# Kernel optimization log

Hardware: AMD Instinct MI355X
Metric: run time of the kernel (lower is better)

The kernel has to match this reference:

```python
import jax, jax.numpy as jnp
import numpy as np

IN_DIM, OUT_DIM = 256, 10
N_EXPERTS, N_MEM, STEPS, N_SUB, MAX_K = 12, 32, 6, 5, 5
EXPERT_DIMS = [2048, 2560, 3072, 3584, 4096, 2304, 2816, 3328, 3840, 4608, 3072, 4096]
MAX_E = 4608
N_ITEMS = 4096
SCALE = IN_DIM ** -0.5

def _gelu(x):
    return jax.nn.gelu(x, approximate=False)

_ACTS = [jax.nn.silu, _gelu, lambda x: x * jnp.tanh(jax.nn.softplus(x)), jax.nn.relu,
         jax.nn.selu, jnp.tanh, jax.nn.softplus, jax.nn.elu]
EXPERT_ACTS = [_ACTS[i % 8] for i in range(N_EXPERTS)]

def _ln(x, s, b, eps=1e-5):
    mu = jnp.mean(x, -1, keepdims=True)
    var = jnp.mean((x - mu) ** 2, -1, keepdims=True)
    return (x - mu) * jax.lax.rsqrt(var + eps) * s + b

def _cell(x, ln_s, ln_b, w1, b1, w2, b2):
    h = _gelu(_ln(x, ln_s, ln_b) @ w1.T + b1)
    return x + h @ w2.T + b2

def _ctx_attn(cur, bank, qw, kw, vw):
    q = cur @ qw.T
    k = bank @ kw.T
    v = bank @ vw.T
    attn = jax.nn.softmax(jnp.einsum('nd,ntd->nt', q, k) * SCALE, axis=-1)
    return jnp.einsum('nt,ntd->nd', attn, v)

def _renorm_sparse_topk(probs, active_k):
    tv, ti = jax.lax.top_k(probs, MAX_K)
    mask = (jnp.arange(MAX_K)[None, :] < active_k[:, None]).astype(probs.dtype)
    vals = tv * mask
    rows = jnp.arange(probs.shape[0])[:, None]
    sparse = jnp.zeros_like(probs).at[rows, ti].set(vals)
    return sparse / jnp.maximum(jnp.sum(sparse, -1, keepdims=True), 1e-6)

def _fwd(x, W, b,
         shared_up_w, shared_down_w, shared_ln_s, shared_ln_b, shared_scale,
         mem_keys, mem_vals, mem_q_w, mem_out_w, mem_wg_w, mem_wg_b, mem_wv_w, mem_wv_b,
         depth_q_w, depth_k_w, depth_v_w, depth_out_w,
         rc_ln_s, rc_ln_b, rc_w1, rc_b1, rc_w2, rc_b2,
         ssm_in_w, ssm_out_w, ssm_decay,
         sub_w, sub_b, gate_w, gate_b,
         budget_w, budget_b,
         exp_up, exp_down, exp_ln_s, exp_ln_b,
         halt_w, halt_b,
         aux_up_w, aux_down_w, aux_ln_s, aux_ln_b, aux_gate_w, aux_gate_b,
         rf_ln_s, rf_ln_b, rf_w1, rf_b1, rf_w2, rf_b2, reflect_out_w,
         coll_q_w, coll_k_w, coll_v_w, coll_out_w,
         revisit_w, revisit_b,
         vc_ln_s, vc_ln_b, vc_w1, vc_b1, vc_w2, vc_b2,
         ver_q_w, ver_k_w, ver_v_w, ver_out_w, ver_gate_w, ver_gate_b, correction_out_w,
         mix):
    n = x.shape[0]
    base = x @ W.T + b
    shared = _ln(jax.nn.silu(x @ shared_up_w.T) @ shared_down_w.T, shared_ln_s, shared_ln_b)
    aux = _ln(_gelu(x @ aux_up_w.T) @ aux_down_w.T, aux_ln_s, aux_ln_b)

    mem_vals_b = jnp.broadcast_to(mem_vals[None], (n, N_MEM, IN_DIM))
    current = x
    mem_logits = jnp.zeros_like(base)
    depth_logits = jnp.zeros_like(base)
    cum_halt = jnp.zeros((n, 1), x.dtype)
    bank = []
    for s in range(STEPS):
        q = current @ mem_q_w.T
        attn = jax.nn.softmax((q @ mem_keys.T) * SCALE, axis=-1)
        mem_read = jnp.einsum('ns,nsd->nd', attn, mem_vals_b)
        wg = jax.nn.sigmoid(jnp.concatenate([current, mem_read], -1) @ mem_wg_w.T + mem_wg_b)
        wv = current @ mem_wv_w.T + mem_wv_b
        mem_vals_b = mem_vals_b * (1.0 - wg[..., None]) + wg[..., None] * wv[:, None, :]
        if bank:
            depth_ctx = _ctx_attn(current, jnp.stack(bank, 1), depth_q_w, depth_k_w, depth_v_w)
        else:
            depth_ctx = jnp.zeros_like(current)
        current = _cell(current + mem_read + depth_ctx,
                        rc_ln_s[s], rc_ln_b[s], rc_w1[s], rc_b1[s], rc_w2[s], rc_b2[s])
        h = jnp.tanh(current @ ssm_in_w.T) * jax.nn.sigmoid(ssm_decay)
        current = current + h @ ssm_out_w.T
        bank.append(current)
        halt = jax.nn.sigmoid((current @ halt_w[s])[:, None] + halt_b[s])
        w_step = (1.0 - cum_halt) * halt
        mem_logits = mem_logits + w_step * (mem_read @ mem_out_w.T)
        depth_logits = depth_logits + w_step * (depth_ctx @ depth_out_w.T)
        cum_halt = jnp.minimum(cum_halt + halt, 1.0)

    sub_logits = jnp.einsum('nd,sed->nse', current, sub_w) + sub_b
    sub_probs = jax.nn.softmax(sub_logits, axis=-1)
    gate = jax.nn.softmax(current @ gate_w.T + gate_b, axis=-1)
    probs = jnp.einsum('ns,nse->ne', gate, sub_probs)
    active_k = jnp.argmax(current @ budget_w.T + budget_b, axis=-1) + 1
    sparse = _renorm_sparse_topk(probs, active_k)

    expert_out = jnp.zeros_like(base)
    for i in range(N_EXPERTS):
        h = EXPERT_ACTS[i](current @ exp_up[i].T)
        o = _ln(h @ exp_down[i].T, exp_ln_s[i], exp_ln_b[i])
        expert_out = expert_out + sparse[:, i:i + 1] * o

    r = current
    for i in range(3):
        r = _cell(r, rf_ln_s[i], rf_ln_b[i], rf_w1[i], rf_b1[i], rf_w2[i], rf_b2[i])
    reflect_logits = r @ reflect_out_w.T

    stack = jnp.stack(bank, 1)
    coll_ctx = _ctx_attn(current, stack, coll_q_w, coll_k_w, coll_v_w)
    coll_logits = coll_ctx @ coll_out_w.T
    revisit = jax.nn.sigmoid(jnp.concatenate([x, current, coll_ctx], -1) @ revisit_w.T + revisit_b)

    v = current
    for i in range(2):
        v = _cell(v, vc_ln_s[i], vc_ln_b[i], vc_w1[i], vc_b1[i], vc_w2[i], vc_b2[i])
    ver_ctx = _ctx_attn(v, stack, ver_q_w, ver_k_w, ver_v_w)
    vg = jax.nn.softmax(jnp.concatenate([v, ver_ctx], -1) @ ver_gate_w.T + ver_gate_b, axis=-1)
    ver_logits = ver_ctx @ ver_out_w.T
    corr_logits = v @ correction_out_w.T

    ag = jax.nn.softmax(x @ aux_gate_w.T + aux_gate_b, axis=-1)
    alpha, beta, gamma, delta, eps_, zeta = [jnp.tanh(mix[i]) for i in range(6)]
    logits = (base
              + shared_scale * (ag[:, :1] * shared + ag[:, 1:] * aux)
              + alpha * expert_out
              + beta * mem_logits + zeta * depth_logits
              + gamma * reflect_logits
              + delta * revisit * coll_logits
              + eps_ * (vg[:, :1] * ver_logits + vg[:, 1:] * corr_logits))
    return logits


def setup_inputs() -> dict:
    key = jax.random.key(0)
    ks = iter(jax.random.split(key, 128))
    def nrm(shape, std=0.02):
        return jax.random.normal(next(ks), shape, jnp.float32) * std
    d, o = IN_DIM, OUT_DIM
    inp = dict(
        x=jax.random.normal(next(ks), (N_ITEMS, d), jnp.float32),
        W=nrm((o, d), 0.05), b=jnp.zeros((o,), jnp.float32),
        shared_up_w=nrm((3072, d)), shared_down_w=nrm((o, 3072)),
        shared_ln_s=jnp.ones((o,)), shared_ln_b=jnp.zeros((o,)),
        shared_scale=jnp.float32(1.0),
        mem_keys=nrm((N_MEM, d)), mem_vals=nrm((N_MEM, d)),
        mem_q_w=nrm((d, d), 0.01), mem_out_w=nrm((o, d), 0.01),
        mem_wg_w=nrm((N_MEM, 2 * d), 0.01), mem_wg_b=jnp.zeros((N_MEM,)),
        mem_wv_w=nrm((d, d), 0.01), mem_wv_b=jnp.zeros((d,)),
        depth_q_w=nrm((d, d), 0.01), depth_k_w=nrm((d, d), 0.01),
        depth_v_w=nrm((d, d), 0.01), depth_out_w=nrm((o, d), 0.01),
        rc_ln_s=jnp.ones((STEPS, d)), rc_ln_b=jnp.zeros((STEPS, d)),
        rc_w1=nrm((STEPS, 896, d)), rc_b1=jnp.zeros((STEPS, 896)),
        rc_w2=nrm((STEPS, d, 896)), rc_b2=jnp.zeros((STEPS, d)),
        ssm_in_w=nrm((48, d)), ssm_out_w=nrm((d, 48)), ssm_decay=jnp.zeros((48,)),
        sub_w=nrm((N_SUB, N_EXPERTS, d)), sub_b=jnp.zeros((N_SUB, N_EXPERTS)),
        gate_w=nrm((N_SUB, d)), gate_b=jnp.zeros((N_SUB,)),
        budget_w=nrm((MAX_K, d), 0.01), budget_b=jnp.zeros((MAX_K,)),
        halt_w=nrm((STEPS, d), 0.01), halt_b=jnp.full((STEPS,), -2.0, jnp.float32),
        aux_up_w=nrm((4096, d)), aux_down_w=nrm((o, 4096)),
        aux_ln_s=jnp.ones((o,)), aux_ln_b=jnp.zeros((o,)),
        aux_gate_w=nrm((2, d), 0.01), aux_gate_b=jnp.zeros((2,)),
        rf_ln_s=jnp.ones((3, d)), rf_ln_b=jnp.zeros((3, d)),
        rf_w1=nrm((3, 1280, d)), rf_b1=jnp.zeros((3, 1280)),
        rf_w2=nrm((3, d, 1280)), rf_b2=jnp.zeros((3, d)),
        reflect_out_w=nrm((o, d), 0.01),
        coll_q_w=nrm((d, d), 0.01), coll_k_w=nrm((d, d), 0.01),
        coll_v_w=nrm((d, d), 0.01), coll_out_w=nrm((o, d), 0.01),
        revisit_w=nrm((1, 3 * d), 0.01), revisit_b=jnp.zeros((1,)),
        vc_ln_s=jnp.ones((2, d)), vc_ln_b=jnp.zeros((2, d)),
        vc_w1=nrm((2, 1536, d)), vc_b1=jnp.zeros((2, 1536)),
        vc_w2=nrm((2, d, 1536)), vc_b2=jnp.zeros((2, d)),
        ver_q_w=nrm((d, d), 0.01), ver_k_w=nrm((d, d), 0.01),
        ver_v_w=nrm((d, d), 0.01), ver_out_w=nrm((o, d), 0.01),
        ver_gate_w=nrm((2, 2 * d), 0.01), ver_gate_b=jnp.zeros((2,)),
        correction_out_w=nrm((o, d), 0.01),
        mix=jnp.full((6,), 0.5, jnp.float32),
    )
    up = jax.random.normal(next(ks), (N_EXPERTS, MAX_E, d), jnp.float32) * 0.02
    down = jax.random.normal(next(ks), (N_EXPERTS, o, MAX_E), jnp.float32) * 0.01
    col = jnp.arange(MAX_E)
    dims = jnp.array(EXPERT_DIMS)
    mask = (col[None, :] < dims[:, None]).astype(jnp.float32)
    inp['exp_up'] = up * mask[:, :, None]
    inp['exp_down'] = down * mask[:, None, :]
    inp['exp_ln_s'] = jnp.ones((N_EXPERTS, o))
    inp['exp_ln_b'] = jnp.zeros((N_EXPERTS, o))
    return inp


def reference(x, W, b,
              shared_up_w, shared_down_w, shared_ln_s, shared_ln_b, shared_scale,
              mem_keys, mem_vals, mem_q_w, mem_out_w, mem_wg_w, mem_wg_b, mem_wv_w, mem_wv_b,
              depth_q_w, depth_k_w, depth_v_w, depth_out_w,
              rc_ln_s, rc_ln_b, rc_w1, rc_b1, rc_w2, rc_b2,
              ssm_in_w, ssm_out_w, ssm_decay,
              sub_w, sub_b, gate_w, gate_b,
              budget_w, budget_b,
              exp_up, exp_down, exp_ln_s, exp_ln_b,
              halt_w, halt_b,
              aux_up_w, aux_down_w, aux_ln_s, aux_ln_b, aux_gate_w, aux_gate_b,
              rf_ln_s, rf_ln_b, rf_w1, rf_b1, rf_w2, rf_b2, reflect_out_w,
              coll_q_w, coll_k_w, coll_v_w, coll_out_w,
              revisit_w, revisit_b,
              vc_ln_s, vc_ln_b, vc_w1, vc_b1, vc_w2, vc_b2,
              ver_q_w, ver_k_w, ver_v_w, ver_out_w, ver_gate_w, ver_gate_b, correction_out_w,
              mix):
    return _fwd(x, W, b,
                shared_up_w, shared_down_w, shared_ln_s, shared_ln_b, shared_scale,
                mem_keys, mem_vals, mem_q_w, mem_out_w, mem_wg_w, mem_wg_b, mem_wv_w, mem_wv_b,
                depth_q_w, depth_k_w, depth_v_w, depth_out_w,
                rc_ln_s, rc_ln_b, rc_w1, rc_b1, rc_w2, rc_b2,
                ssm_in_w, ssm_out_w, ssm_decay,
                sub_w, sub_b, gate_w, gate_b,
                budget_w, budget_b,
                exp_up, exp_down, exp_ln_s, exp_ln_b,
                halt_w, halt_b,
                aux_up_w, aux_down_w, aux_ln_s, aux_ln_b, aux_gate_w, aux_gate_b,
                rf_ln_s, rf_ln_b, rf_w1, rf_b1, rf_w2, rf_b2, reflect_out_w,
                coll_q_w, coll_k_w, coll_v_w, coll_out_w,
                revisit_w, revisit_b,
                vc_ln_s, vc_ln_b, vc_w1, vc_b1, vc_w2, vc_b2,
                ver_q_w, ver_k_w, ver_v_w, ver_out_w, ver_gate_w, ver_gate_b, correction_out_w,
                mix)
```

## Files before the change

### kernel.cpp

```cpp
#include <hip/hip_runtime.h>


constexpr int NI      = 4096;
constexpr int DIM     = 256;
constexpr int ODIM    = 10;
constexpr int NMEM_   = 32;
constexpr int NSTEPS_ = 6;
constexpr int NEXPERT_= 12;
constexpr int MAXE    = 4608;
constexpr int TOTCOL  = 46592;
#define SCL 0.0625f

__constant__ int GCNT[14] = {8,10,12,14,16,9,11,13,15,18,12,16,12,16};
__constant__ int CCNT[14] = {32,40,48,56,64,36,44,52,60,72,48,64,48,64};
__constant__ int ZCOL[14] = {0,2048,4608,7680,11264,15360,17664,20480,
                             23808,27648,32256,35328,39424,42496};

typedef __attribute__((ext_vector_type(8))) short short8v;
typedef __attribute__((ext_vector_type(4))) float float4v;
typedef __attribute__((ext_vector_type(4))) unsigned short ushort4v;


__device__ __forceinline__ float wred_sum(float v){
  #pragma unroll
  for (int m = 32; m > 0; m >>= 1) v += __shfl_xor(v, m, 64);
  return v;
}
__device__ __forceinline__ float wred_max(float v){
  #pragma unroll
  for (int m = 32; m > 0; m >>= 1) v = fmaxf(v, __shfl_xor(v, m, 64));
  return v;
// ... 7 lines not shown
    case 1: return geluf(x);
    case 2: return x*tanhf(softplusf(x));
    case 3: return fmaxf(x,0.f);
    case 4: { const float l=1.0507009873554805f, al=1.6732632423543772f;
              return x>0.f ? l*x : l*al*expm1f(x); }
    case 5: return tanhf(x);
    case 6: return softplusf(x);
    default: return x>0.f ? x : expm1f(x);
  }
}
__device__ __forceinline__ unsigned short f2b(float f){
  unsigned u = __float_as_uint(f);
  u = u + 0x7FFFu + ((u >> 16) & 1u);
  return (unsigned short)(u >> 16);
}
__device__ __forceinline__ float dot256f(const float* __restrict__ a,
                                         const float* __restrict__ w, float s){
  for (int k = 0; k < DIM; k += 4){
    float4 av = *(const float4*)&a[k];
    float4 wv = *(const float4*)&w[k];
    s = fmaf(av.x,wv.x, fmaf(av.y,wv.y, fmaf(av.z,wv.z, fmaf(av.w,wv.w, s))));
  }
  return s;
}
__device__ __forceinline__ void ln10(const float* p, const float* s, const float* b, float* o){
  float mu = 0.f;
  #pragma unroll
  for (int i=0;i<ODIM;i++) mu += p[i];
  mu *= 0.1f;
  float var = 0.f;
// ... 32 lines not shown
  int t = threadIdx.x;
  int c = t >> 3, kb = (t & 7)*32;
  const float* srow = src + (size_t)(colbase + c)*DIM + kb;
  #pragma unroll
  for (int j = 0; j < 4; j++){
    float4 f0 = *(const float4*)&srow[j*8];
    float4 f1 = *(const float4*)&srow[j*8+4];
    short8v s;
    s[0]=(short)f2b(f0.x); s[1]=(short)f2b(f0.y); s[2]=(short)f2b(f0.z); s[3]=(short)f2b(f0.w);
    s[4]=(short)f2b(f1.x); s[5]=(short)f2b(f1.y); s[6]=(short)f2b(f1.z); s[7]=(short)f2b(f1.w);
    int kq = (t & 7)*4 + j;
    *(short8v*)&dst[((size_t)kq*64 + c)*8] = s;
  }
}

template<int EPI>
__global__ __launch_bounds__(256)
void gemm_k(const float* __restrict__ A, const float* __restrict__ W,
            const float* __restrict__ bias, const float* __restrict__ R,
            float* __restrict__ C, int N, int K)
{
  __shared__ float As[32][68];
  __shared__ float Ws[32][68];
  const int bm = blockIdx.y*64, bn = blockIdx.x*64;
  const int tid = threadIdx.x;
  const int tx = tid & 15, ty = tid >> 4;
  const int lrow = tid >> 2, lkq = (tid & 3) * 8;
  float acc[4][4] = {};
  for (int k0 = 0; k0 < K; k0 += 32){
    #pragma unroll
    for (int h = 0; h < 2; ++h){
      int kk = lkq + h*4;
      float4 va = make_float4(0.f,0.f,0.f,0.f), vw = make_float4(0.f,0.f,0.f,0.f);
      if (k0 + kk < K)
        va = *(const float4*)&A[(size_t)(bm+lrow)*K + k0 + kk];
      if (bn + lrow < N && k0 + kk < K)
        vw = *(const float4*)&W[(size_t)(bn+lrow)*K + k0 + kk];
      As[kk+0][lrow]=va.x; As[kk+1][lrow]=va.y; As[kk+2][lrow]=va.z; As[kk+3][lrow]=va.w;
      Ws[kk+0][lrow]=vw.x; Ws[kk+1][lrow]=vw.y; Ws[kk+2][lrow]=vw.z; Ws[kk+3][lrow]=vw.w;
    }
    __syncthreads();
    #pragma unroll
    for (int kk = 0; kk < 32; ++kk){
      float4 a4 = *(const float4*)&As[kk][ty*4];
      float4 b4 = *(const float4*)&Ws[kk][tx*4];
      float av[4] = {a4.x,a4.y,a4.z,a4.w};
      float bv[4] = {b4.x,b4.y,b4.z,b4.w};
      #pragma unroll
      for (int i=0;i<4;i++)
        #pragma unroll
        for (int j=0;j<4;j++) acc[i][j] = fmaf(av[i], bv[j], acc[i][j]);
    }
    __syncthreads();
  }
  #pragma unroll
  for (int i=0;i<4;i++){
    int r = bm + ty*4 + i;
    #pragma unroll
    for (int j=0;j<4;j++){
      int c = bn + tx*4 + j;
      if (c >= N) continue;
      float v = acc[i][j];
      if constexpr (EPI==1) v += bias[c];
      else if constexpr (EPI==2) v = geluf(v + bias[c]);
      else if constexpr (EPI==3) v = v + bias[c] + R[(size_t)r*N + c];
      C[(size_t)r*N + c] = v;
    }
  }
}

template<int EPI>
__global__ __launch_bounds__(256)
void bgemm_k(const short* __restrict__ A, const short* __restrict__ B,
             const float* __restrict__ bias, const float* __restrict__ R,
             float* __restrict__ Cf, unsigned short* __restrict__ Cb,
             int N, int K)
{
  __shared__ short As[128][40];
  __shared__ short Bsm[64][40];
  const int bm = blockIdx.y*128, bn = blockIdx.x*64;
  const int tid = threadIdx.x;
// ... 35 lines not shown
      for (int reg = 0; reg < 4; reg++){
        int row = bm + wave*32 + mt*16 + lg*4 + reg;
        int col = bn + nt*16 + l15;
        float v = acc[mt][nt][reg];
        if constexpr (EPI==0){
          v = geluf(v + bias[col]);
          Cb[(size_t)row*N + col] = f2b(v);
        } else {
          v = v + bias[col] + R[(size_t)row*N + col];
          Cf[(size_t)row*N + col] = v;
        }
      }
}

__global__ __launch_bounds__(512)
void moe2_k(const float* __restrict__ cur, const float* __restrict__ x,
            const float* __restrict__ exp_up, const float* __restrict__ shared_up,
            const float* __restrict__ aux_up, const short* __restrict__ upb,
            const float* __restrict__ exp_down, const float* __restrict__ shared_down,
            const float* __restrict__ aux_down,
            float* __restrict__ expert_pre, float* __restrict__ shared_pre,
            float* __restrict__ aux_pre)
{
  __shared__ short Bs[16384];
  __shared__ float Ds[64][12];
  int gy = blockIdx.y, z = 0;
  while (gy >= GCNT[z]){ gy -= GCNT[z]; z++; }
  const int localcol = gy*256;
  int act, dstride; const float* upf; const float* down; float* outp;
  if (z < NEXPERT_){
    act = z & 7;
    upf = exp_up + (size_t)z*MAXE*DIM;
    down = exp_down + (size_t)z*ODIM*MAXE; dstride = MAXE;
    outp = expert_pre + (size_t)z*NI*ODIM;
  } else if (z == NEXPERT_){
    act = 0; upf = shared_up; down = shared_down; dstride = 3072; outp = shared_pre;
  } else {
    act = 1; upf = aux_up; down = aux_down; dstride = 4096; outp = aux_pre;
  }
  const float* X = (z < NEXPERT_) ? cur : x;
  const int bm = blockIdx.x*128;
  const int tid = threadIdx.x, wave = tid >> 6, lane = tid & 63;
  const int l15 = lane & 15, lg = lane >> 4;

  short8v afrag[8];
  {
    const float* xr = X + (size_t)(bm + wave*16 + l15)*DIM;
    #pragma unroll
    for (int ks = 0; ks < 8; ks++){
      float4 v0 = *(const float4*)&xr[ks*32 + lg*8];
      float4 v1 = *(const float4*)&xr[ks*32 + lg*8 + 4];
      short8v a;
      a[0]=(short)f2b(v0.x); a[1]=(short)f2b(v0.y); a[2]=(short)f2b(v0.z); a[3]=(short)f2b(v0.w);
      a[4]=(short)f2b(v1.x); a[5]=(short)f2b(v1.y); a[6]=(short)f2b(v1.z); a[7]=(short)f2b(v1.w);
      afrag[ks] = a;
    }
  }
  float racc[4][10];
  #pragma unroll
  for (int r = 0; r < 4; r++)
    #pragma unroll
    for (int o = 0; o < 10; o++) racc[r][o] = 0.f;

  const int sc = tid & 63, sw = tid >> 6;
  const int gchunk0 = (ZCOL[z] + localcol) >> 6;
  for (int ch = 0; ch < 4; ch++){
    const int cb = localcol + ch*64;
    __syncthreads();
    if (upb){
      const short* chunk = upb + ((size_t)(gchunk0 + ch))*16384;
      #pragma unroll
      for (int i = 0; i < 4; i++){
        int u = tid + 512*i;
        short8v v = *(const short8v*)&chunk[(size_t)u*8];
        int c = u & 63, kq = u >> 6;
        int byteoff = ((c << 9) + (kq << 4)) ^ ((c & 7) << 4);
        *(short8v*)((char*)Bs + byteoff) = v;
      }
    } else {
      const float* srow = upf + (size_t)(cb + sc)*DIM;
      #pragma unroll
      for (int i = 0; i < 4; i++){
        int kq = sw + 8*i;
        float4 f0 = *(const float4*)&srow[kq*8];
        float4 f1 = *(const float4*)&srow[kq*8 + 4];
        short8v s;
        s[0]=(short)f2b(f0.x); s[1]=(short)f2b(f0.y); s[2]=(short)f2b(f0.z); s[3]=(short)f2b(f0.w);
        s[4]=(short)f2b(f1.x); s[5]=(short)f2b(f1.y); s[6]=(short)f2b(f1.z); s[7]=(short)f2b(f1.w);
        int byteoff = ((sc << 9) + (kq << 4)) ^ ((sc & 7) << 4);
        *(short8v*)((char*)Bs + byteoff) = s;
      }
    }
    for (int t2 = tid; t2 < 640; t2 += 512){
      int e = t2 & 63, o = t2 >> 6;
      Ds[e][o] = down[(size_t)o*dstride + cb + e];
    }
    __syncthreads();

    float4v acc[4] = {};
    #pragma unroll
    for (int ks = 0; ks < 8; ks++){
      #pragma unroll
      for (int nt = 0; nt < 4; nt++){
        int c = nt*16 + l15, kq = ks*4 + lg;
        int byteoff = ((c << 9) + (kq << 4)) ^ ((c & 7) << 4);
        short8v b = *(const short8v*)((const char*)Bs + byteoff);
        acc[nt] = __builtin_amdgcn_mfma_f32_16x16x32_bf16(afrag[ks], b, acc[nt], 0, 0, 0);
      }
    }
    #pragma unroll
    for (int nt = 0; nt < 4; nt++){
      const float* dp = &Ds[nt*16 + l15][0];
      float4 d0 = *(const float4*)dp;
      float4 d1 = *(const float4*)(dp + 4);
      float  d8 = dp[8], d9 = dp[9];
      float dv[10] = {d0.x,d0.y,d0.z,d0.w,d1.x,d1.y,d1.z,d1.w,d8,d9};
      float hv[4];
      #pragma unroll
      for (int reg = 0; reg < 4; reg++) hv[reg] = act_apply(act, acc[nt][reg]);
      #pragma unroll
      for (int o = 0; o < 10; o++)
        #pragma unroll
        for (int reg = 0; reg < 4; reg++)
          racc[reg][o] = fmaf(hv[reg], dv[o], racc[reg][o]);
    }
  }
  #pragma unroll
  for (int reg = 0; reg < 4; reg++)
    #pragma unroll
    for (int o = 0; o < 10; o++){
      float v = racc[reg][o];
      v += __shfl_xor(v, 1, 64); v += __shfl_xor(v, 2, 64);
      v += __shfl_xor(v, 4, 64); v += __shfl_xor(v, 8, 64);
      racc[reg][o] = v;
    }
  if (l15 == 0){
    #pragma unroll
    for (int reg = 0; reg < 4; reg++){
      int row = bm + wave*16 + lg*4 + reg;
      #pragma unroll
      for (int o = 0; o < 10; o++)
        atomicAdd(&outp[(size_t)row*ODIM + o], racc[reg][o]);
    }
  }
}

__global__ void atb_k(const float* __restrict__ A, const float* __restrict__ B,
                      float* __restrict__ C, int M, int I, int J)
{
  int idx = blockIdx.x*256 + threadIdx.x;
  if (idx >= I*J) return;
  int i = idx / J, j = idx - i*J;
  float s = 0.f;
  for (int m = 0; m < M; m++) s = fmaf(A[(size_t)m*I+i], B[(size_t)m*J+j], s);
  C[idx] = s;
}
__global__ void ab_k(const float* __restrict__ A, const float* __restrict__ B,
                     float* __restrict__ C, int M, int K, int N)
{
// ... 369 lines not shown
  #pragma unroll
  for (int o = 0; o < ODIM; o++){
    size_t ix = (size_t)item*ODIM + o;
    float v = base10[ix]
      + ss*(ag0*sh[o] + ag1*axl[o])
      + al*eo[o]
      + be*mem_logits[ix] + ze*depth_logits[ix]
      + ga*reflect10[ix]
      + de*rv*coll10[ix]
      + ep*(vg0*ver10[ix] + vg1*corr10[ix]);
    out[ix] = v;
  }
}


static void launch_gemm(int epi, const float* A, const float* W, const float* b,
                        const float* R, float* C, int N, int K, hipStream_t stream)
{
  dim3 g((N+63)/64, NI/64), blk(256);
  switch(epi){
    case 0: gemm_k<0><<<g,blk,0,stream>>>(A,W,b,R,C,N,K); break;
    case 1: gemm_k<1><<<g,blk,0,stream>>>(A,W,b,R,C,N,K); break;
    case 2: gemm_k<2><<<g,blk,0,stream>>>(A,W,b,R,C,N,K); break;
    case 3: gemm_k<3><<<g,blk,0,stream>>>(A,W,b,R,C,N,K); break;
  }
}

static void launch_cvt(const float* in, unsigned short* out, size_t n, hipStream_t stream)
{
  cvt_k<<<(unsigned)((n/4 + 255)/256), 256, 0, stream>>>(in, out, (int)n);
}

extern "C" void kernel_launch(void* const* d_in, const int* in_sizes, int n_in,
                              void* d_out, int out_size, void* d_ws, size_t ws_size,
                              hipStream_t stream)
{
  (void)in_sizes; (void)n_in; (void)out_size;
  const float* x             = (const float*)d_in[0];
  const float* Wm            = (const float*)d_in[1];
  const float* bvec          = (const float*)d_in[2];
  const float* shared_up_w   = (const float*)d_in[3];
  const float* shared_down_w = (const float*)d_in[4];
  const float* shared_ln_s   = (const float*)d_in[5];
  const float* shared_ln_b   = (const float*)d_in[6];
  const float* shared_scale  = (const float*)d_in[7];
  const float* mem_keys      = (const float*)d_in[8];
  const float* mem_vals      = (const float*)d_in[9];
  const float* mem_q_w       = (const float*)d_in[10];
  const float* mem_out_w     = (const float*)d_in[11];
  const float* mem_wg_w      = (const float*)d_in[12];
  const float* mem_wg_b      = (const float*)d_in[13];
  const float* mem_wv_w      = (const float*)d_in[14];
// ... 50 lines not shown
  const float* ver_out_w     = (const float*)d_in[65];
  const float* ver_gate_w    = (const float*)d_in[66];
  const float* ver_gate_b    = (const float*)d_in[67];
  const float* correction_out_w = (const float*)d_in[68];
  const float* mix           = (const float*)d_in[69];
  const float* exp_up        = (const float*)d_in[70];
  const float* exp_down      = (const float*)d_in[71];
  const float* exp_ln_s      = (const float*)d_in[72];
  const float* exp_ln_b      = (const float*)d_in[73];
  float* out = (float*)d_out;

  float* w = (float*)d_ws;
  size_t off = 0;
  auto WS = [&](size_t nf){ float* p = w + off; off += nf; return p; };
  float* bank      = WS((size_t)NSTEPS_*NI*DIM);
  float* cur_in    = WS((size_t)NI*DIM);
  float* t_ln      = WS((size_t)NI*DIM);
  float* hbig      = WS((size_t)NI*896);
  float* mem_read  = WS((size_t)NI*DIM);
  float* depth_ctx = WS((size_t)NI*DIM);
  float* q2        = WS((size_t)NI*DIM);
  float* wsumb     = WS((size_t)NI*DIM);
  float* wv_hist   = WS((size_t)NSTEPS_*NI*DIM);
  float* a_state   = WS((size_t)NI*NMEM_);
  float* c_state   = WS((size_t)NI*NMEM_*NSTEPS_);
  float* rbuf      = WS((size_t)NI*DIM);
  float* vbuf      = WS((size_t)NI*DIM);
  float* coll_ctx  = WS((size_t)NI*DIM);
  float* ver_ctx   = WS((size_t)NI*DIM);
  float* sparse    = WS((size_t)NI*NEXPERT_);
  float* base10    = WS((size_t)NI*ODIM);
  float* reflect10 = WS((size_t)NI*ODIM);
  float* coll10    = WS((size_t)NI*ODIM);
  float* ver10     = WS((size_t)NI*ODIM);
  float* corr10    = WS((size_t)NI*ODIM);
  float* PdT       = WS((size_t)DIM*DIM);
  float* PcT       = WS((size_t)DIM*DIM);
  float* PvT       = WS((size_t)DIM*DIM);
  float* MK        = WS((size_t)NMEM_*DIM);
  float* zbase     = w + off;
  float* mem_logits   = WS((size_t)NI*ODIM);
  float* depth_logits = WS((size_t)NI*ODIM);
  float* shared_pre   = WS((size_t)NI*ODIM);
  float* aux_pre      = WS((size_t)NI*ODIM);
  float* expert_pre   = WS((size_t)NEXPERT_*NI*ODIM);
  float* cum_halt     = WS((size_t)NI);
  size_t zbytes = (size_t)((w + off) - zbase) * sizeof(float);
  hipMemsetAsync((void*)zbase, 0, zbytes, stream);

  unsigned short* bb = (unsigned short*)(w + off);
  size_t boff = 0;
  auto BS = [&](size_t ns){ unsigned short* p = bb + boff; boff += ns; return p; };
  unsigned short* t_ln_b = BS((size_t)NI*DIM);
  unsigned short* rfw1b  = BS((size_t)3*1280*DIM);
  unsigned short* rfw2b  = BS((size_t)3*DIM*1280);
  unsigned short* vcw1b  = BS((size_t)2*1536*DIM);
  unsigned short* vcw2b  = BS((size_t)2*DIM*1536);
  unsigned short* upb    = bb + boff;
  size_t upb_n = (size_t)TOTCOL*DIM;
  size_t base_bytes = off*sizeof(float) + boff*sizeof(unsigned short);
  bool use_upb = (ws_size >= base_bytes + upb_n*sizeof(unsigned short));
  unsigned short* hb = (unsigned short*)hbig;

  launch_cvt(rf_w1, rfw1b, (size_t)3*1280*DIM, stream);
  launch_cvt(rf_w2, rfw2b, (size_t)3*DIM*1280, stream);
  launch_cvt(vc_w1, vcw1b, (size_t)2*1536*DIM, stream);
  launch_cvt(vc_w2, vcw2b, (size_t)2*DIM*1536, stream);
  if (use_upb)
    cvtup_k<<<TOTCOL/64, 512, 0, stream>>>(exp_up, shared_up_w, aux_up_w, (short*)upb);

  atb_k<<<(DIM*DIM+255)/256, 256, 0, stream>>>(depth_k_w, depth_q_w, PdT, DIM, DIM, DIM);
  atb_k<<<(DIM*DIM+255)/256, 256, 0, stream>>>(coll_k_w,  coll_q_w,  PcT, DIM, DIM, DIM);
  atb_k<<<(DIM*DIM+255)/256, 256, 0, stream>>>(ver_k_w,   ver_q_w,   PvT, DIM, DIM, DIM);
  ab_k <<<(NMEM_*DIM+255)/256, 256, 0, stream>>>(mem_keys, mem_q_w, MK, NMEM_, DIM, DIM);

  const float* cur = x;
  for (int s = 0; s < NSTEPS_; s++){
    memread2_k<<<NI/4, 256, 0, stream>>>(cur, MK, a_state, c_state, mem_vals,
                                         wv_hist, mem_read, s);
    memwrite_k<<<NI/4, 256, 0, stream>>>(cur, mem_read, mem_wg_w, mem_wg_b,
                                         a_state, c_state, s);
    launch_gemm(1, cur, mem_wv_w, mem_wv_b, nullptr,
                wv_hist + (size_t)s*NI*DIM, DIM, DIM, stream);
    if (s > 0){
      launch_gemm(0, cur, PdT, nullptr, nullptr, q2, DIM, DIM, stream);
      bankattn_k<<<NI/4, 256, 0, stream>>>(q2, bank, wsumb, s);
      launch_gemm(0, wsumb, depth_v_w, nullptr, nullptr, depth_ctx, DIM, DIM, stream);
    }
    ln3_k<<<NI/4, 256, 0, stream>>>(cur, mem_read, (s > 0 ? depth_ctx : nullptr),
                                    rc_ln_s + (size_t)s*DIM, rc_ln_b + (size_t)s*DIM,
                                    cur_in, t_ln, nullptr);
    launch_gemm(2, t_ln, rc_w1 + (size_t)s*896*DIM, rc_b1 + (size_t)s*896,
                nullptr, hbig, 896, DIM, stream);
    launch_gemm(3, hbig, rc_w2 + (size_t)s*DIM*896, rc_b2 + (size_t)s*DIM,
                cur_in, cur_in, DIM, 896, stream);
    float* newcur = bank + (size_t)s*NI*DIM;
    ssmhalt_k<<<NI/4, 256, 0, stream>>>(cur_in, mem_read, depth_ctx,
                                        ssm_in_w, ssm_out_w, ssm_decay,
                                        halt_w, halt_b, mem_out_w, depth_out_w,
                                        newcur, mem_logits, depth_logits, cum_halt, s);
    cur = newcur;
  }

  router2_k<<<NI/4, 256, 0, stream>>>(cur, sub_w, sub_b, gate_w, gate_b,
                                      budget_w, budget_b, sparse);

  moe2_k<<<dim3(NI/128, 182), 512, 0, stream>>>(
      cur, x, exp_up, shared_up_w, aux_up_w, use_upb ? (const short*)upb : nullptr,
      exp_down, shared_down_w, aux_down_w, expert_pre, shared_pre, aux_pre);

  const float* rsrc = cur;
  for (int i = 0; i < 3; i++){
    ln3_k<<<NI/4, 256, 0, stream>>>(rsrc, nullptr, nullptr,
                                    rf_ln_s + (size_t)i*DIM, rf_ln_b + (size_t)i*DIM,
                                    nullptr, nullptr, t_ln_b);
    bgemm_k<0><<<dim3(1280/64, NI/128), 256, 0, stream>>>(
        (const short*)t_ln_b, (const short*)(rfw1b + (size_t)i*1280*DIM),
        rf_b1 + (size_t)i*1280, nullptr, nullptr, hb, 1280, DIM);
    bgemm_k<1><<<dim3(DIM/64, NI/128), 256, 0, stream>>>(
        (const short*)hb, (const short*)(rfw2b + (size_t)i*DIM*1280),
        rf_b2 + (size_t)i*DIM, rsrc, rbuf, nullptr, DIM, 1280);
    rsrc = rbuf;
  }

  const float* vsrc = cur;
  for (int i = 0; i < 2; i++){
    ln3_k<<<NI/4, 256, 0, stream>>>(vsrc, nullptr, nullptr,
                                    vc_ln_s + (size_t)i*DIM, vc_ln_b + (size_t)i*DIM,
                                    nullptr, nullptr, t_ln_b);
    bgemm_k<0><<<dim3(1536/64, NI/128), 256, 0, stream>>>(
        (const short*)t_ln_b, (const short*)(vcw1b + (size_t)i*1536*DIM),
        vc_b1 + (size_t)i*1536, nullptr, nullptr, hb, 1536, DIM);
    bgemm_k<1><<<dim3(DIM/64, NI/128), 256, 0, stream>>>(
        (const short*)hb, (const short*)(vcw2b + (size_t)i*DIM*1536),
        vc_b2 + (size_t)i*DIM, vsrc, vbuf, nullptr, DIM, 1536);
    vsrc = vbuf;
  }

  launch_gemm(0, cur, PcT, nullptr, nullptr, q2, DIM, DIM, stream);
  bankattn_k<<<NI/4, 256, 0, stream>>>(q2, bank, wsumb, NSTEPS_);
  launch_gemm(0, wsumb, coll_v_w, nullptr, nullptr, coll_ctx, DIM, DIM, stream);

  launch_gemm(0, vbuf, PvT, nullptr, nullptr, q2, DIM, DIM, stream);
  bankattn_k<<<NI/4, 256, 0, stream>>>(q2, bank, wsumb, NSTEPS_);
  launch_gemm(0, wsumb, ver_v_w, nullptr, nullptr, ver_ctx, DIM, DIM, stream);

  heads_k<<<(NI*50 + 255)/256, 256, 0, stream>>>(
      rbuf, coll_ctx, ver_ctx, vbuf, x,
      reflect_out_w, coll_out_w, ver_out_w, correction_out_w, Wm, bvec,
      reflect10, coll10, ver10, corr10, base10);

  final_k<<<(NI+255)/256, 256, 0, stream>>>(
      x, cur, vbuf, coll_ctx, ver_ctx,
      base10, shared_pre, aux_pre, expert_pre, sparse,
      mem_logits, depth_logits, reflect10, coll10, ver10, corr10,
      shared_ln_s, shared_ln_b, aux_ln_s, aux_ln_b, exp_ln_s, exp_ln_b,
      aux_gate_w, aux_gate_b, ver_gate_w, ver_gate_b, revisit_w, revisit_b,
      shared_scale, mix, out);
}
```

Before: 3.360 ms.

## Enlarge fp32 GEMM tiles, fuse wv/depth-query GEMMs, pipeline MoE and drop atomics

Replaces the 64x64 fp32 GEMM with a 128-row tiled kernel using 8xTN register blocking. The mem_wv and depth-query projections are fused into one 512-wide GEMM over concatenated weights. The MoE kernel now reads pre-converted bf16 activations, always uses the bf16 up-weight buffer, and double-buffers chunk loads in registers. Its atomicAdd accumulation is replaced by bf16 partial sums plus a separate reduction kernel. The workspace is reorganised so buffers overlap, which risks aliasing, and storing partials in bf16 loses some precision.

```diff
diff --git a/kernel.cpp b/kernel.cpp
--- a/kernel.cpp
+++ b/kernel.cpp
@@ -9,12 +9,14 @@
 constexpr int NEXPERT_= 12;
 constexpr int MAXE    = 4608;
 constexpr int TOTCOL  = 46592;
+constexpr int NGRP    = 182;
 #define SCL 0.0625f
 
-__constant__ int GCNT[14] = {8,10,12,14,16,9,11,13,15,18,12,16,12,16};
-__constant__ int CCNT[14] = {32,40,48,56,64,36,44,52,60,72,48,64,48,64};
-__constant__ int ZCOL[14] = {0,2048,4608,7680,11264,15360,17664,20480,
-                             23808,27648,32256,35328,39424,42496};
+__constant__ int GCNT[14]   = {8,10,12,14,16,9,11,13,15,18,12,16,12,16};
+__constant__ int GSTART[14] = {0,8,18,30,44,60,69,80,93,108,126,138,154,166};
+__constant__ int CCNT[14]   = {32,40,48,56,64,36,44,52,60,72,48,64,48,64};
+__constant__ int ZCOL[14]   = {0,2048,4608,7680,11264,15360,17664,20480,
+                               23808,27648,32256,35328,39424,42496};
 
 typedef __attribute__((ext_vector_type(8))) short short8v;
 typedef __attribute__((ext_vector_type(4))) float float4v;
@@ -52,6 +54,9 @@
   u = u + 0x7FFFu + ((u >> 16) & 1u);
   return (unsigned short)(u >> 16);
 }
+__device__ __forceinline__ float b2f(unsigned short u){
+  return __uint_as_float((unsigned)u << 16);
+}
 __device__ __forceinline__ float dot256f(const float* __restrict__ a,
                                          const float* __restrict__ w, float s){
   for (int k = 0; k < DIM; k += 4){
@@ -114,57 +119,85 @@
   }
 }
 
-template<int EPI>
+template<int EPI, int BN>
 __global__ __launch_bounds__(256)
-void gemm_k(const float* __restrict__ A, const float* __restrict__ W,
-            const float* __restrict__ bias, const float* __restrict__ R,
-            float* __restrict__ C, int N, int K)
-{
-  __shared__ float As[32][68];
-  __shared__ float Ws[32][68];
-  const int bm = blockIdx.y*64, bn = blockIdx.x*64;
+void gemm128_k(const float* __restrict__ A, const float* __restrict__ W,
+               const float* __restrict__ bias, const float* __restrict__ R,
+               float* __restrict__ C, float* __restrict__ C2, int N, int K)
+{
+  __shared__ float As[32][132];
+  __shared__ float Bs[32][BN==128?132:68];
+  const int bm = blockIdx.y*128, bn = blockIdx.x*BN;
   const int tid = threadIdx.x;
   const int tx = tid & 15, ty = tid >> 4;
-  const int lrow = tid >> 2, lkq = (tid & 3) * 8;
-  float acc[4][4] = {};
+  constexpr int TN = BN/16;
+  float acc[8][TN] = {};
+  const int arow = tid >> 1, ak = (tid & 1)*16;
+  const int brow = tid >> 2, bk = (tid & 3)*8;
   for (int k0 = 0; k0 < K; k0 += 32){
-    #pragma unroll
-    for (int h = 0; h < 2; ++h){
-      int kk = lkq + h*4;
-      float4 va = make_float4(0.f,0.f,0.f,0.f), vw = make_float4(0.f,0.f,0.f,0.f);
-      if (k0 + kk < K)
-        va = *(const float4*)&A[(size_t)(bm+lrow)*K + k0 + kk];
-      if (bn + lrow < N && k0 + kk < K)
-        vw = *(const float4*)&W[(size_t)(bn+lrow)*K + k0 + kk];
-      As[kk+0][lrow]=va.x; As[kk+1][lrow]=va.y; As[kk+2][lrow]=va.z; As[kk+3][lrow]=va.w;
-      Ws[kk+0][lrow]=vw.x; Ws[kk+1][lrow]=vw.y; Ws[kk+2][lrow]=vw.z; Ws[kk+3][lrow]=vw.w;
+    float4 a[4];
+    #pragma unroll
+    for (int i=0;i<4;i++) a[i] = *(const float4*)&A[(size_t)(bm+arow)*K + k0 + ak + 4*i];
+    float4 b[4];
+    if constexpr (BN==128){
+      #pragma unroll
+      for (int i=0;i<4;i++) b[i] = *(const float4*)&W[(size_t)(bn+arow)*K + k0 + ak + 4*i];
+    } else {
+      #pragma unroll
+      for (int i=0;i<2;i++) b[i] = *(const float4*)&W[(size_t)(bn+brow)*K + k0 + bk + 4*i];
     }
     __syncthreads();
     #pragma unroll
-    for (int kk = 0; kk < 32; ++kk){
-      float4 a4 = *(const float4*)&As[kk][ty*4];
-      float4 b4 = *(const float4*)&Ws[kk][tx*4];
-      float av[4] = {a4.x,a4.y,a4.z,a4.w};
-      float bv[4] = {b4.x,b4.y,b4.z,b4.w};
-      #pragma unroll
-      for (int i=0;i<4;i++)
+    for (int i=0;i<4;i++){
+      As[ak+4*i+0][arow]=a[i].x; As[ak+4*i+1][arow]=a[i].y;
+      As[ak+4*i+2][arow]=a[i].z; As[ak+4*i+3][arow]=a[i].w;
+    }
+    if constexpr (BN==128){
+      #pragma unroll
+      for (int i=0;i<4;i++){
+        Bs[ak+4*i+0][arow]=b[i].x; Bs[ak+4*i+1][arow]=b[i].y;
+        Bs[ak+4*i+2][arow]=b[i].z; Bs[ak+4*i+3][arow]=b[i].w;
+      }
+    } else {
+      #pragma unroll
+      for (int i=0;i<2;i++){
+        Bs[bk+4*i+0][brow]=b[i].x; Bs[bk+4*i+1][brow]=b[i].y;
+        Bs[bk+4*i+2][brow]=b[i].z; Bs[bk+4*i+3][brow]=b[i].w;
+      }
+    }
+    __syncthreads();
+    #pragma unroll
+    for (int kk=0;kk<32;kk++){
+      float a8[8];
+      *(float4*)&a8[0] = *(const float4*)&As[kk][ty*8];
+      *(float4*)&a8[4] = *(const float4*)&As[kk][ty*8+4];
+      float b8[TN];
+      if constexpr (TN==8){
+        *(float4*)&b8[0] = *(const float4*)&Bs[kk][tx*8];
+        *(float4*)&b8[4] = *(const float4*)&Bs[kk][tx*8+4];
+      } else {
+        *(float4*)&b8[0] = *(const float4*)&Bs[kk][tx*4];
+      }
+      #pragma unroll
+      for (int i=0;i<8;i++)
         #pragma unroll
-        for (int j=0;j<4;j++) acc[i][j] = fmaf(av[i], bv[j], acc[i][j]);
-    }
-    __syncthreads();
-  }
-  #pragma unroll
-  for (int i=0;i<4;i++){
-    int r = bm + ty*4 + i;
-    #pragma unroll
-    for (int j=0;j<4;j++){
-      int c = bn + tx*4 + j;
-      if (c >= N) continue;
+        for (int j=0;j<TN;j++) acc[i][j] = fmaf(a8[i], b8[j], acc[i][j]);
+    }
+  }
+  #pragma unroll
+  for (int i=0;i<8;i++){
+    int r = bm + ty*8 + i;
+    #pragma unroll
+    for (int j=0;j<TN;j++){
+      int c = bn + tx*TN + j;
       float v = acc[i][j];
-      if constexpr (EPI==1) v += bias[c];
-      else if constexpr (EPI==2) v = geluf(v + bias[c]);
-      else if constexpr (EPI==3) v = v + bias[c] + R[(size_t)r*N + c];
-      C[(size_t)r*N + c] = v;
+      if constexpr (EPI==0){ C[(size_t)r*N + c] = v; }
+      else if constexpr (EPI==2){ C[(size_t)r*N + c] = geluf(v + bias[c]); }
+      else if constexpr (EPI==3){ C[(size_t)r*N + c] = v + bias[c] + R[(size_t)r*N + c]; }
+      else if constexpr (EPI==6){
+        if (c < 256) C[(size_t)r*256 + c] = v + bias[c];
+        else C2[(size_t)r*256 + (c-256)] = v;
+      }
     }
   }
 }
@@ -230,47 +263,32 @@
 }
 
 __global__ __launch_bounds__(512)
-void moe2_k(const float* __restrict__ cur, const float* __restrict__ x,
-            const float* __restrict__ exp_up, const float* __restrict__ shared_up,
-            const float* __restrict__ aux_up, const short* __restrict__ upb,
+void moe3_k(const unsigned short* __restrict__ curb, const unsigned short* __restrict__ xb,
+            const short* __restrict__ upb,
             const float* __restrict__ exp_down, const float* __restrict__ shared_down,
             const float* __restrict__ aux_down,
-            float* __restrict__ expert_pre, float* __restrict__ shared_pre,
-            float* __restrict__ aux_pre)
+            unsigned short* __restrict__ part)
 {
   __shared__ short Bs[16384];
   __shared__ float Ds[64][12];
-  int gy = blockIdx.y, z = 0;
+  const int g = blockIdx.y;
+  int gy = g, z = 0;
   while (gy >= GCNT[z]){ gy -= GCNT[z]; z++; }
   const int localcol = gy*256;
-  int act, dstride; const float* upf; const float* down; float* outp;
-  if (z < NEXPERT_){
-    act = z & 7;
-    upf = exp_up + (size_t)z*MAXE*DIM;
-    down = exp_down + (size_t)z*ODIM*MAXE; dstride = MAXE;
-    outp = expert_pre + (size_t)z*NI*ODIM;
-  } else if (z == NEXPERT_){
-    act = 0; upf = shared_up; down = shared_down; dstride = 3072; outp = shared_pre;
-  } else {
-    act = 1; upf = aux_up; down = aux_down; dstride = 4096; outp = aux_pre;
-  }
-  const float* X = (z < NEXPERT_) ? cur : x;
+  int act, dstride; const float* down;
+  if (z < 12){ act = z & 7; down = exp_down + (size_t)z*ODIM*MAXE; dstride = MAXE; }
+  else if (z == 12){ act = 0; down = shared_down; dstride = 3072; }
+  else { act = 1; down = aux_down; dstride = 4096; }
+  const unsigned short* X = (z < 12) ? curb : xb;
   const int bm = blockIdx.x*128;
   const int tid = threadIdx.x, wave = tid >> 6, lane = tid & 63;
   const int l15 = lane & 15, lg = lane >> 4;
 
   short8v afrag[8];
-  {
-    const float* xr = X + (size_t)(bm + wave*16 + l15)*DIM;
-    #pragma unroll
-    for (int ks = 0; ks < 8; ks++){
-      float4 v0 = *(const float4*)&xr[ks*32 + lg*8];
-      float4 v1 = *(const float4*)&xr[ks*32 + lg*8 + 4];
-      short8v a;
-      a[0]=(short)f2b(v0.x); a[1]=(short)f2b(v0.y); a[2]=(short)f2b(v0.z); a[3]=(short)f2b(v0.w);
-      a[4]=(short)f2b(v1.x); a[5]=(short)f2b(v1.y); a[6]=(short)f2b(v1.z); a[7]=(short)f2b(v1.w);
-      afrag[ks] = a;
-    }
+  { const unsigned short* xr = X + (size_t)(bm + wave*16 + l15)*DIM;
+    #pragma unroll
+    for (int ks = 0; ks < 8; ks++)
+      afrag[ks] = *(const short8v*)&xr[ks*32 + lg*8];
   }
   float racc[4][10];
   #pragma unroll
@@ -278,44 +296,44 @@
     #pragma unroll
     for (int o = 0; o < 10; o++) racc[r][o] = 0.f;
 
-  const int sc = tid & 63, sw = tid >> 6;
   const int gchunk0 = (ZCOL[z] + localcol) >> 6;
+  const int dso = tid >> 6, dse = tid & 63;
+
+  auto ld = [&](int ch, short8v* p, float& d0, float& d1){
+    const short* chunk = upb + ((size_t)(gchunk0 + ch))*16384;
+    #pragma unroll
+    for (int i = 0; i < 4; i++)
+      p[i] = *(const short8v*)&chunk[(size_t)(tid + 512*i)*8];
+    int cb = localcol + ch*64;
+    d0 = down[(size_t)dso*dstride + cb + dse];
+    d1 = (tid < 128) ? down[(size_t)(dso+8)*dstride + cb + dse] : 0.f;
+  };
+
+  short8v preA[4], preB[4];
+  float dA0, dA1, dB0, dB1;
+  ld(0, preA, dA0, dA1);
+  #pragma unroll
   for (int ch = 0; ch < 4; ch++){
-    const int cb = localcol + ch*64;
+    const short8v* P = (ch & 1) ? preB : preA;
+    float d0 = (ch & 1) ? dB0 : dA0;
+    float d1 = (ch & 1) ? dB1 : dA1;
+    #pragma unroll
+    for (int i = 0; i < 4; i++){
+      int u = tid + 512*i;
+      int c = u & 63, kq = u >> 6;
+      int byteoff = ((c << 9) + (kq << 4)) ^ ((c & 7) << 4);
+      *(short8v*)((char*)Bs + byteoff) = P[i];
+    }
+    Ds[dse][dso] = d0;
+    if (tid < 128) Ds[dse][dso + 8] = d1;
     __syncthreads();
-    if (upb){
-      const short* chunk = upb + ((size_t)(gchunk0 + ch))*16384;
-      #pragma unroll
-      for (int i = 0; i < 4; i++){
-        int u = tid + 512*i;
-        short8v v = *(const short8v*)&chunk[(size_t)u*8];
-        int c = u & 63, kq = u >> 6;
-        int byteoff = ((c << 9) + (kq << 4)) ^ ((c & 7) << 4);
-        *(short8v*)((char*)Bs + byteoff) = v;
-      }
-    } else {
-      const float* srow = upf + (size_t)(cb + sc)*DIM;
-      #pragma unroll
-      for (int i = 0; i < 4; i++){
-        int kq = sw + 8*i;
-        float4 f0 = *(const float4*)&srow[kq*8];
-        float4 f1 = *(const float4*)&srow[kq*8 + 4];
-        short8v s;
-        s[0]=(short)f2b(f0.x); s[1]=(short)f2b(f0.y); s[2]=(short)f2b(f0.z); s[3]=(short)f2b(f0.w);
-        s[4]=(short)f2b(f1.x); s[5]=(short)f2b(f1.y); s[6]=(short)f2b(f1.z); s[7]=(short)f2b(f1.w);
-        int byteoff = ((sc << 9) + (kq << 4)) ^ ((sc & 7) << 4);
-        *(short8v*)((char*)Bs + byteoff) = s;
-      }
-    }
-    for (int t2 = tid; t2 < 640; t2 += 512){
-      int e = t2 & 63, o = t2 >> 6;
-      Ds[e][o] = down[(size_t)o*dstride + cb + e];
-    }
-    __syncthreads();
-
+    if (ch < 3){
+      if (ch & 1) ld(ch + 1, preA, dA0, dA1);
+      else        ld(ch + 1, preB, dB0, dB1);
+    }
     float4v acc[4] = {};
     #pragma unroll
-    for (int ks = 0; ks < 8; ks++){
+    for (int ks = 0; ks < 8; ks++)
       #pragma unroll
       for (int nt = 0; nt < 4; nt++){
         int c = nt*16 + l15, kq = ks*4 + lg;
@@ -323,14 +341,13 @@
         short8v b = *(const short8v*)((const char*)Bs + byteoff);
         acc[nt] = __builtin_amdgcn_mfma_f32_16x16x32_bf16(afrag[ks], b, acc[nt], 0, 0, 0);
       }
-    }
     #pragma unroll
     for (int nt = 0; nt < 4; nt++){
       const float* dp = &Ds[nt*16 + l15][0];
-      float4 d0 = *(const float4*)dp;
-      float4 d1 = *(const float4*)(dp + 4);
+      float4 dv0 = *(const float4*)dp;
+      float4 dv1 = *(const float4*)(dp + 4);
       float  d8 = dp[8], d9 = dp[9];
-      float dv[10] = {d0.x,d0.y,d0.z,d0.w,d1.x,d1.y,d1.z,d1.w,d8,d9};
+      float dv[10] = {dv0.x,dv0.y,dv0.z,dv0.w,dv1.x,dv1.y,dv1.z,dv1.w,d8,d9};
       float hv[4];
       #pragma unroll
       for (int reg = 0; reg < 4; reg++) hv[reg] = act_apply(act, acc[nt][reg]);
@@ -340,6 +357,7 @@
         for (int reg = 0; reg < 4; reg++)
           racc[reg][o] = fmaf(hv[reg], dv[o], racc[reg][o]);
     }
+    __syncthreads();
   }
   #pragma unroll
   for (int reg = 0; reg < 4; reg++)
@@ -356,9 +374,25 @@
       int row = bm + wave*16 + lg*4 + reg;
       #pragma unroll
       for (int o = 0; o < 10; o++)
-        atomicAdd(&outp[(size_t)row*ODIM + o], racc[reg][o]);
-    }
-  }
+        part[((size_t)g*NI + row)*ODIM + o] = f2b(racc[reg][o]);
+    }
+  }
+}
+
+__global__ __launch_bounds__(256)
+void red_k(const unsigned short* __restrict__ part, float* __restrict__ expert_pre,
+           float* __restrict__ shared_pre, float* __restrict__ aux_pre)
+{
+  int idx = blockIdx.x*256 + threadIdx.x;
+  if (idx >= 14*NI*ODIM) return;
+  int z = idx / (NI*ODIM), rem = idx - z*NI*ODIM;
+  float s = 0.f;
+  int g0 = GSTART[z], gn = GCNT[z];
+  for (int g2 = 0; g2 < gn; g2++)
+    s += b2f(part[(size_t)(g0 + g2)*NI*ODIM + rem]);
+  if (z < 12) expert_pre[(size_t)z*NI*ODIM + rem] = s;
+  else if (z == 12) shared_pre[rem] = s;
+  else aux_pre[rem] = s;
 }
 
 __global__ void atb_k(const float* __restrict__ A, const float* __restrict__ B,
@@ -758,18 +792,6 @@
 }
 
 
-static void launch_gemm(int epi, const float* A, const float* W, const float* b,
-                        const float* R, float* C, int N, int K, hipStream_t stream)
-{
-  dim3 g((N+63)/64, NI/64), blk(256);
-  switch(epi){
-    case 0: gemm_k<0><<<g,blk,0,stream>>>(A,W,b,R,C,N,K); break;
-    case 1: gemm_k<1><<<g,blk,0,stream>>>(A,W,b,R,C,N,K); break;
-    case 2: gemm_k<2><<<g,blk,0,stream>>>(A,W,b,R,C,N,K); break;
-    case 3: gemm_k<3><<<g,blk,0,stream>>>(A,W,b,R,C,N,K); break;
-  }
-}
-
 static void launch_cvt(const float* in, unsigned short* out, size_t n, hipStream_t stream)
 {
   cvt_k<<<(unsigned)((n/4 + 255)/256), 256, 0, stream>>>(in, out, (int)n);
@@ -779,7 +801,7 @@
                               void* d_out, int out_size, void* d_ws, size_t ws_size,
                               hipStream_t stream)
 {
-  (void)in_sizes; (void)n_in; (void)out_size;
+  (void)in_sizes; (void)n_in; (void)out_size; (void)ws_size;
   const float* x             = (const float*)d_in[0];
   const float* Wm            = (const float*)d_in[1];
   const float* bvec          = (const float*)d_in[2];
@@ -860,62 +882,56 @@
   size_t off = 0;
   auto WS = [&](size_t nf){ float* p = w + off; off += nf; return p; };
   float* bank      = WS((size_t)NSTEPS_*NI*DIM);
-  float* cur_in    = WS((size_t)NI*DIM);
-  float* t_ln      = WS((size_t)NI*DIM);
-  float* hbig      = WS((size_t)NI*896);
-  float* mem_read  = WS((size_t)NI*DIM);
-  float* depth_ctx = WS((size_t)NI*DIM);
-  float* q2        = WS((size_t)NI*DIM);
-  float* wsumb     = WS((size_t)NI*DIM);
-  float* wv_hist   = WS((size_t)NSTEPS_*NI*DIM);
-  float* a_state   = WS((size_t)NI*NMEM_);
-  float* c_state   = WS((size_t)NI*NMEM_*NSTEPS_);
   float* rbuf      = WS((size_t)NI*DIM);
   float* vbuf      = WS((size_t)NI*DIM);
   float* coll_ctx  = WS((size_t)NI*DIM);
   float* ver_ctx   = WS((size_t)NI*DIM);
+  float* q2        = WS((size_t)NI*DIM);
+  float* wsumb     = WS((size_t)NI*DIM);
   float* sparse    = WS((size_t)NI*NEXPERT_);
   float* base10    = WS((size_t)NI*ODIM);
   float* reflect10 = WS((size_t)NI*ODIM);
   float* coll10    = WS((size_t)NI*ODIM);
   float* ver10     = WS((size_t)NI*ODIM);
   float* corr10    = WS((size_t)NI*ODIM);
-  float* PdT       = WS((size_t)DIM*DIM);
   float* PcT       = WS((size_t)DIM*DIM);
   float* PvT       = WS((size_t)DIM*DIM);
   float* MK        = WS((size_t)NMEM_*DIM);
+  float* Wvq       = WS((size_t)512*DIM);
+  float* expert_pre= WS((size_t)NEXPERT_*NI*ODIM);
+  float* shared_pre= WS((size_t)NI*ODIM);
+  float* aux_pre   = WS((size_t)NI*ODIM);
+  unsigned short* cur_b = (unsigned short*)WS((size_t)NI*DIM/2);
+  unsigned short* x_b   = (unsigned short*)WS((size_t)NI*DIM/2);
   float* zbase     = w + off;
   float* mem_logits   = WS((size_t)NI*ODIM);
   float* depth_logits = WS((size_t)NI*ODIM);
-  float* shared_pre   = WS((size_t)NI*ODIM);
-  float* aux_pre      = WS((size_t)NI*ODIM);
-  float* expert_pre   = WS((size_t)NEXPERT_*NI*ODIM);
   float* cum_halt     = WS((size_t)NI);
   size_t zbytes = (size_t)((w + off) - zbase) * sizeof(float);
   hipMemsetAsync((void*)zbase, 0, zbytes, stream);
 
-  unsigned short* bb = (unsigned short*)(w + off);
-  size_t boff = 0;
-  auto BS = [&](size_t ns){ unsigned short* p = bb + boff; boff += ns; return p; };
-  unsigned short* t_ln_b = BS((size_t)NI*DIM);
-  unsigned short* rfw1b  = BS((size_t)3*1280*DIM);
-  unsigned short* rfw2b  = BS((size_t)3*DIM*1280);
-  unsigned short* vcw1b  = BS((size_t)2*1536*DIM);
-  unsigned short* vcw2b  = BS((size_t)2*DIM*1536);
-  unsigned short* upb    = bb + boff;
-  size_t upb_n = (size_t)TOTCOL*DIM;
-  size_t base_bytes = off*sizeof(float) + boff*sizeof(unsigned short);
-  bool use_upb = (ws_size >= base_bytes + upb_n*sizeof(unsigned short));
-  unsigned short* hb = (unsigned short*)hbig;
-
-  launch_cvt(rf_w1, rfw1b, (size_t)3*1280*DIM, stream);
-  launch_cvt(rf_w2, rfw2b, (size_t)3*DIM*1280, stream);
-  launch_cvt(vc_w1, vcw1b, (size_t)2*1536*DIM, stream);
-  launch_cvt(vc_w2, vcw2b, (size_t)2*DIM*1536, stream);
-  if (use_upb)
-    cvtup_k<<<TOTCOL/64, 512, 0, stream>>>(exp_up, shared_up_w, aux_up_w, (short*)upb);
-
-  atb_k<<<(DIM*DIM+255)/256, 256, 0, stream>>>(depth_k_w, depth_q_w, PdT, DIM, DIM, DIM);
+  float* U = w + off;
+  float* wv_hist   = U;
+  float* hbig      = U + (size_t)NSTEPS_*NI*DIM;
+  float* cur_in    = hbig + (size_t)NI*896;
+  float* t_ln      = cur_in + (size_t)NI*DIM;
+  float* mem_read  = t_ln + (size_t)NI*DIM;
+  float* depth_ctx = mem_read + (size_t)NI*DIM;
+  float* a_state   = depth_ctx + (size_t)NI*DIM;
+  float* c_state   = a_state + (size_t)NI*NMEM_;
+  unsigned short* upb    = (unsigned short*)U;
+  unsigned short* hb     = (unsigned short*)U;
+  float* ovl = U + 5963776;
+  unsigned short* t_ln_b = (unsigned short*)ovl;          ovl += 524288;
+  unsigned short* rfw1b  = (unsigned short*)ovl;          ovl += 491520;
+  unsigned short* rfw2b  = (unsigned short*)ovl;          ovl += 491520;
+  unsigned short* vcw1b  = (unsigned short*)ovl;          ovl += 393216;
+  unsigned short* vcw2b  = (unsigned short*)ovl;          ovl += 393216;
+  unsigned short* part   = (unsigned short*)ovl;
+
+  hipMemcpyAsync(Wvq, mem_wv_w, (size_t)DIM*DIM*sizeof(float),
+                 hipMemcpyDeviceToDevice, stream);
+  atb_k<<<(DIM*DIM+255)/256, 256, 0, stream>>>(depth_k_w, depth_q_w, Wvq + (size_t)DIM*DIM, DIM, DIM, DIM);
   atb_k<<<(DIM*DIM+255)/256, 256, 0, stream>>>(coll_k_w,  coll_q_w,  PcT, DIM, DIM, DIM);
   atb_k<<<(DIM*DIM+255)/256, 256, 0, stream>>>(ver_k_w,   ver_q_w,   PvT, DIM, DIM, DIM);
   ab_k <<<(NMEM_*DIM+255)/256, 256, 0, stream>>>(mem_keys, mem_q_w, MK, NMEM_, DIM, DIM);
@@ -926,20 +942,22 @@
                                          wv_hist, mem_read, s);
     memwrite_k<<<NI/4, 256, 0, stream>>>(cur, mem_read, mem_wg_w, mem_wg_b,
                                          a_state, c_state, s);
-    launch_gemm(1, cur, mem_wv_w, mem_wv_b, nullptr,
-                wv_hist + (size_t)s*NI*DIM, DIM, DIM, stream);
+    gemm128_k<6,128><<<dim3(4, NI/128), 256, 0, stream>>>(
+        cur, Wvq, mem_wv_b, nullptr, wv_hist + (size_t)s*NI*DIM, q2, 512, DIM);
     if (s > 0){
-      launch_gemm(0, cur, PdT, nullptr, nullptr, q2, DIM, DIM, stream);
       bankattn_k<<<NI/4, 256, 0, stream>>>(q2, bank, wsumb, s);
-      launch_gemm(0, wsumb, depth_v_w, nullptr, nullptr, depth_ctx, DIM, DIM, stream);
+      gemm128_k<0,64><<<dim3(4, NI/128), 256, 0, stream>>>(
+          wsumb, depth_v_w, nullptr, nullptr, depth_ctx, nullptr, DIM, DIM);
     }
     ln3_k<<<NI/4, 256, 0, stream>>>(cur, mem_read, (s > 0 ? depth_ctx : nullptr),
                                     rc_ln_s + (size_t)s*DIM, rc_ln_b + (size_t)s*DIM,
                                     cur_in, t_ln, nullptr);
-    launch_gemm(2, t_ln, rc_w1 + (size_t)s*896*DIM, rc_b1 + (size_t)s*896,
-                nullptr, hbig, 896, DIM, stream);
-    launch_gemm(3, hbig, rc_w2 + (size_t)s*DIM*896, rc_b2 + (size_t)s*DIM,
-                cur_in, cur_in, DIM, 896, stream);
+    gemm128_k<2,128><<<dim3(7, NI/128), 256, 0, stream>>>(
+        t_ln, rc_w1 + (size_t)s*896*DIM, rc_b1 + (size_t)s*896, nullptr,
+        hbig, nullptr, 896, DIM);
+    gemm128_k<3,64><<<dim3(4, NI/128), 256, 0, stream>>>(
+        hbig, rc_w2 + (size_t)s*DIM*896, rc_b2 + (size_t)s*DIM, cur_in,
+        cur_in, nullptr, DIM, 896);
     float* newcur = bank + (size_t)s*NI*DIM;
     ssmhalt_k<<<NI/4, 256, 0, stream>>>(cur_in, mem_read, depth_ctx,
                                         ssm_in_w, ssm_out_w, ssm_decay,
@@ -951,9 +969,17 @@
   router2_k<<<NI/4, 256, 0, stream>>>(cur, sub_w, sub_b, gate_w, gate_b,
                                       budget_w, budget_b, sparse);
 
-  moe2_k<<<dim3(NI/128, 182), 512, 0, stream>>>(
-      cur, x, exp_up, shared_up_w, aux_up_w, use_upb ? (const short*)upb : nullptr,
-      exp_down, shared_down_w, aux_down_w, expert_pre, shared_pre, aux_pre);
+  launch_cvt(cur, cur_b, (size_t)NI*DIM, stream);
+  launch_cvt(x,   x_b,   (size_t)NI*DIM, stream);
+  cvtup_k<<<TOTCOL/64, 512, 0, stream>>>(exp_up, shared_up_w, aux_up_w, (short*)upb);
+  launch_cvt(rf_w1, rfw1b, (size_t)3*1280*DIM, stream);
+  launch_cvt(rf_w2, rfw2b, (size_t)3*DIM*1280, stream);
+  launch_cvt(vc_w1, vcw1b, (size_t)2*1536*DIM, stream);
+  launch_cvt(vc_w2, vcw2b, (size_t)2*DIM*1536, stream);
+
+  moe3_k<<<dim3(NI/128, NGRP), 512, 0, stream>>>(
+      cur_b, x_b, (const short*)upb, exp_down, shared_down_w, aux_down_w, part);
+  red_k<<<(14*NI*ODIM + 255)/256, 256, 0, stream>>>(part, expert_pre, shared_pre, aux_pre);
 
   const float* rsrc = cur;
   for (int i = 0; i < 3; i++){
@@ -983,13 +1009,17 @@
     vsrc = vbuf;
   }
 
-  launch_gemm(0, cur, PcT, nullptr, nullptr, q2, DIM, DIM, stream);
+  gemm128_k<0,64><<<dim3(4, NI/128), 256, 0, stream>>>(
+      cur, PcT, nullptr, nullptr, q2, nullptr, DIM, DIM);
   bankattn_k<<<NI/4, 256, 0, stream>>>(q2, bank, wsumb, NSTEPS_);
-  launch_gemm(0, wsumb, coll_v_w, nullptr, nullptr, coll_ctx, DIM, DIM, stream);
-
-  launch_gemm(0, vbuf, PvT, nullptr, nullptr, q2, DIM, DIM, stream);
+  gemm128_k<0,64><<<dim3(4, NI/128), 256, 0, stream>>>(
+      wsumb, coll_v_w, nullptr, nullptr, coll_ctx, nullptr, DIM, DIM);
+
+  gemm128_k<0,64><<<dim3(4, NI/128), 256, 0, stream>>>(
+      vbuf, PvT, nullptr, nullptr, q2, nullptr, DIM, DIM);
   bankattn_k<<<NI/4, 256, 0, stream>>>(q2, bank, wsumb, NSTEPS_);
-  launch_gemm(0, wsumb, ver_v_w, nullptr, nullptr, ver_ctx, DIM, DIM, stream);
+  gemm128_k<0,64><<<dim3(4, NI/128), 256, 0, stream>>>(
+      wsumb, ver_v_w, nullptr, nullptr, ver_ctx, nullptr, DIM, DIM);
 
   heads_k<<<(NI*50 + 255)/256, 256, 0, stream>>>(
       rbuf, coll_ctx, ver_ctx, vbuf, x,
```

After: 3.507 ms. 4.4% more time.
